# Kernel optimization log

Hardware: AMD Instinct MI355X
Metric: run time of the kernel (lower is better)

The kernel has to match this reference:

```python
import jax, jax.numpy as jnp
import numpy as np

NUM_HEADS = 16
TOP_K = 128
LN_EPS = 1e-5


def layernorm(x, w, b):
    mu = jnp.mean(x, axis=-1, keepdims=True)
    var = jnp.mean((x - mu) ** 2, axis=-1, keepdims=True)
    return (x - mu) * jax.lax.rsqrt(var + LN_EPS) * w + b


def top_k_activation(x, k):
    # keep top-k along last dim, zero elsewhere (scatter, like torch.scatter_)
    n = x.shape[-1]
    if k >= n:
        return x
    vals, idx = jax.lax.top_k(x, k)
    flat = x.reshape(-1, n)
    rows = jnp.arange(flat.shape[0])[:, None]
    out = jnp.zeros_like(flat).at[rows, idx.reshape(-1, k)].set(vals.reshape(-1, k))
    return out.reshape(x.shape)


def setup_inputs() -> dict:
    key = jax.random.key(0)
    ks = jax.random.split(key, 8)
    B, S, H = 2, 2048, 1024
    hd = H // NUM_HEADS
    return {
        "x": jax.random.normal(ks[0], (B, S, H), dtype=jnp.float32),
        "W_Q": jax.random.normal(ks[1], (H, H), dtype=jnp.float32) * 0.02,
        "W_K": jax.random.normal(ks[2], (H, H), dtype=jnp.float32) * 0.02,
        "W_V": jax.random.normal(ks[3], (H, H), dtype=jnp.float32) * 0.02,
        "W_O": jax.random.normal(ks[4], (H, H), dtype=jnp.float32) * 0.02,
        "q_ln_w": jnp.ones((hd,), dtype=jnp.float32),
        "q_ln_b": jnp.zeros((hd,), dtype=jnp.float32),
        "k_ln_w": jnp.ones((hd,), dtype=jnp.float32),
        "k_ln_b": jnp.zeros((hd,), dtype=jnp.float32),
        "sparse_W_V": jax.random.normal(ks[5], (NUM_HEADS, hd, TOP_K), dtype=jnp.float32) * 0.02,
        "sparse_W_O": jax.random.normal(ks[6], (NUM_HEADS, TOP_K, hd), dtype=jnp.float32) * 0.02,
    }


def reference(x, W_Q, W_K, W_V, W_O, q_ln_w, q_ln_b, k_ln_w, k_ln_b, sparse_W_V, sparse_W_O):
    B, S, H = x.shape
    nh = sparse_W_V.shape[0]
    hd = H // nh
    # projections (torch Linear: x @ W.T)
    def split_heads(t):
        return t.reshape(B, S, nh, hd).transpose(0, 2, 1, 3)  # [B, nh, S, hd]
    Q = split_heads(jnp.einsum('bsd,od->bso', x, W_Q))
    K = split_heads(jnp.einsum('bsd,od->bso', x, W_K))
    V = split_heads(jnp.einsum('bsd,od->bso', x, W_V))
    Q = layernorm(Q, q_ln_w, q_ln_b)
    K = layernorm(K, k_ln_w, k_ln_b)
    scores = jnp.einsum('bhqd,bhkd->bhqk', Q, K) / jnp.sqrt(jnp.float32(hd))
    attn = jax.nn.softmax(scores, axis=-1)
    context = jnp.einsum('bhqk,bhkd->bhqd', attn, V)  # [B, nh, S, hd]
    # faithful to source: transpose then reshape mixes batch/seq/head dims
    context_flat = context.transpose(0, 2, 1, 3).reshape(B * nh, S, hd)
    v_weights = sparse_W_V.mean(axis=2)  # [nh, hd]
    z = jnp.einsum('bnd,hd->bhn', context_flat, v_weights)  # [B*nh, nh, S]
    z_sparse = top_k_activation(z, TOP_K)  # top-k along seq axis, as in source
    o_weights = sparse_W_O.mean(axis=1)  # [nh, hd]
    y_flat = jnp.einsum('bhn,hd->bnd', z_sparse, o_weights)  # [B*nh, S, hd]
    y = y_flat.reshape(B, nh, S, hd).transpose(0, 2, 1, 3).reshape(B, S, H)
    y = jnp.einsum('bsd,od->bso', y, W_O)
    return y
```

## Files before the change

kernel.cpp:

```cpp
#include <hip/hip_runtime.h>
#include <math.h>

#define NB   2
#define SEQ  2048
#define NHD  16
#define HDD  64
#define HID  1024
#define TOPK 128

__global__ void k_prep_means(const float* __restrict__ sWV, const float* __restrict__ sWO,
                             double* __restrict__ vw, double* __restrict__ ow) {
  int t = threadIdx.x;
  for (int o = t; o < NHD * HDD; o += 256) {
    const float* p = sWV + (size_t)o * TOPK;
    double s = 0.0;
    for (int i = 0; i < TOPK; i++) s += (double)p[i];
    vw[o] = s * (1.0 / 128.0);
    int h = o >> 6, d = o & 63;
    const float* q = sWO + ((size_t)h * TOPK) * HDD + d;
    double s2 = 0.0;
    for (int i = 0; i < TOPK; i++) s2 += (double)q[(size_t)i * HDD];
    ow[o] = s2 * (1.0 / 128.0);
  }
}

__global__ void k_prep_wvp_g(const float* __restrict__ W_V, const float* __restrict__ W_O,
                             const double* __restrict__ vw, const double* __restrict__ ow,
                             double* __restrict__ WVP, float* __restrict__ G) {
  int blk = blockIdx.x;
  int t = threadIdx.x;
  if (blk < 256) {
    int n = blk >> 4, h = blk & 15;
    for (int j = t; j < HID; j += 256) {
      double s = 0.0;
      for (int d = 0; d < 64; d++)
        s += (double)W_V[(size_t)(n * 64 + d) * HID + j] * vw[h * 64 + d];
      WVP[(size_t)blk * HID + j] = s;
    }
  } else {
    int r = blk - 256;
    int m = r >> 4, h = r & 15;
    for (int o = t; o < HID; o += 256) {
      double s = 0.0;
      for (int d = 0; d < 64; d++)
        s += ow[h * 64 + d] * (double)W_O[(size_t)o * HID + m * 64 + d];
      G[(size_t)r * HID + o] = (float)s;
    }
  }
}

__global__ __launch_bounds__(256) void k_proj_qk(
    const float* __restrict__ x, const float* __restrict__ W_Q, const float* __restrict__ W_K,
    const float* __restrict__ qw, const float* __restrict__ qb,
    const float* __restrict__ kw, const float* __restrict__ kb,
    double* __restrict__ Qh, double* __restrict__ Kh) {
  __shared__ float  AsT[32][68];
  __shared__ float  BsT[32][68];
  __shared__ double Cs[64][65];
  __shared__ double red[64][4];

  int rt = blockIdx.x, ot = blockIdx.y;
  bool isQ = (ot < 16);
  const float* W = isQ ? W_Q : W_K;
  int head = isQ ? ot : ot - 16;
  int o0 = head * 64;
  int t = threadIdx.x;
  int tr = t >> 4, tc = t & 15;

  double acc[4][4];
  #pragma unroll
  for (int i = 0; i < 4; i++)
    #pragma unroll
    for (int j = 0; j < 4; j++) acc[i][j] = 0.0;

  for (int k0 = 0; k0 < HID; k0 += 32) {
    #pragma unroll
    for (int i = 0; i < 8; i++) {
      int idx = t + i * 256;
      int r = idx >> 5, c = idx & 31;
      AsT[c][r] = x[(size_t)(rt * 64 + r) * HID + k0 + c];
      BsT[c][r] = W[(size_t)(o0 + r) * HID + k0 + c];
    }
    __syncthreads();
    #pragma unroll 1
    for (int kk = 0; kk < 32; kk++) {
      float4 af = *(const float4*)&AsT[kk][tr * 4];
      float4 bf = *(const float4*)&BsT[kk][tc * 4];
      double a[4], b[4];
      a[0] = (double)af.x; a[1] = (double)af.y; a[2] = (double)af.z; a[3] = (double)af.w;
      b[0] = (double)bf.x; b[1] = (double)bf.y; b[2] = (double)bf.z; b[3] = (double)bf.w;
      #pragma unroll
      for (int i = 0; i < 4; i++)
        #pragma unroll
        for (int j = 0; j < 4; j++) acc[i][j] = fma(a[i], b[j], acc[i][j]);
    }
    __syncthreads();
  }

  #pragma unroll
  for (int i = 0; i < 4; i++)
    #pragma unroll
    for (int j = 0; j < 4; j++) Cs[tr * 4 + i][tc * 4 + j] = acc[i][j];
  __syncthreads();

  int r = t >> 2, p = t & 3;
  double s = 0.0;
  for (int i = 0; i < 16; i++) s += Cs[r][p * 16 + i];
  red[r][p] = s;
  __syncthreads();
  double mu = (red[r][0] + red[r][1] + red[r][2] + red[r][3]) * (1.0 / 64.0);
  __syncthreads();
  double s2 = 0.0;
  for (int i = 0; i < 16; i++) { double dl = Cs[r][p * 16 + i] - mu; s2 += dl * dl; }
  red[r][p] = s2;
  __syncthreads();
  double var = (red[r][0] + red[r][1] + red[r][2] + red[r][3]) * (1.0 / 64.0);
  double inv = 1.0 / sqrt(var + 1e-5);

  int R = rt * 64 + r;
  int b = R >> 11, ss = R & 2047;
  const float* lw = isQ ? qw : kw;
  const float* lb = isQ ? qb : kb;
  double* outp = isQ ? Qh : Kh;
  size_t base = (((size_t)b * 16 + head) * SEQ + ss) * 64;
  for (int i = 0; i < 16; i++) {
    int d = p * 16 + i;
    outp[base + d] = (Cs[r][d] - mu) * inv * (double)lw[d] + (double)lb[d];
  }
}

__global__ __launch_bounds__(256) void k_proj_vp(
    const float* __restrict__ x, const double* __restrict__ WVP, double* __restrict__ Vp) {
  __shared__ float  AsT[32][68];
  __shared__ double BsT[32][68];
  int rt = blockIdx.x, ot = blockIdx.y;
  int t = threadIdx.x, tr = t >> 4, tc = t & 15;

  double acc[4][4];
  #pragma unroll
  for (int i = 0; i < 4; i++)
    #pragma unroll
    for (int j = 0; j < 4; j++) acc[i][j] = 0.0;

  for (int k0 = 0; k0 < HID; k0 += 32) {
    #pragma unroll
    for (int i = 0; i < 8; i++) {
      int idx = t + i * 256;
      int r = idx >> 5, c = idx & 31;
      AsT[c][r] = x[(size_t)(rt * 64 + r) * HID + k0 + c];
      BsT[c][r] = WVP[(size_t)(ot * 64 + r) * HID + k0 + c];
    }
    __syncthreads();
    #pragma unroll 1
    for (int kk = 0; kk < 32; kk++) {
      float4 af = *(const float4*)&AsT[kk][tr * 4];
      double2 b01 = *(const double2*)&BsT[kk][tc * 4];
      double2 b23 = *(const double2*)&BsT[kk][tc * 4 + 2];
      double a[4], b[4];
      a[0] = (double)af.x; a[1] = (double)af.y; a[2] = (double)af.z; a[3] = (double)af.w;
      b[0] = b01.x; b[1] = b01.y; b[2] = b23.x; b[3] = b23.y;
      #pragma unroll
      for (int i = 0; i < 4; i++)
        #pragma unroll
        for (int j = 0; j < 4; j++) acc[i][j] = fma(a[i], b[j], acc[i][j]);
    }
    __syncthreads();
  }
  #pragma unroll
  for (int i = 0; i < 4; i++) {
    int R = rt * 64 + tr * 4 + i;
    int b = R >> 11, k = R & 2047;
    #pragma unroll
    for (int j = 0; j < 4; j++) {
      int cc = ot * 64 + tc * 4 + j;
      int n = cc >> 4, h = cc & 15;
      Vp[((((size_t)b * 16 + n) * SEQ) + k) * 16 + h] = acc[i][j];
    }
  }
}

__global__ __launch_bounds__(256, 2) void k_attn(
    const double* __restrict__ Qh, const double* __restrict__ Kh,
    const double* __restrict__ Vp, double* __restrict__ pnum, double* __restrict__ pden) {
  int kh = blockIdx.x;
  int qt = blockIdx.y;
  int bn = blockIdx.z;
  int t = threadIdx.x;
  int s = qt * 256 + t;
  int kspan = SEQ / gridDim.x;

  __shared__ double2 K2[64][32];
  __shared__ double2 V2[64][8];

  double2 q2[32];
  const double2* qp = (const double2*)(Qh + ((size_t)bn * SEQ + s) * 64);
  #pragma unroll
  for (int d = 0; d < 32; d++) q2[d] = qp[d];

  double2 num2[8];
  #pragma unroll
  for (int i = 0; i < 8; i++) { num2[i].x = 0.0; num2[i].y = 0.0; }
  double den = 0.0;

  int k0 = kh * kspan;
  for (int kc = 0; kc < kspan; kc += 64) {
    const double2* kb = (const double2*)(Kh + ((size_t)bn * SEQ + k0 + kc) * 64);
    #pragma unroll
    for (int i = 0; i < 8; i++) {
      int idx = t + i * 256;
      K2[idx >> 5][idx & 31] = kb[idx];
    }
    const double2* vb = (const double2*)(Vp + ((size_t)bn * SEQ + k0 + kc) * 16);
    #pragma unroll
    for (int i = 0; i < 2; i++) {
      int idx = t + i * 256;
      V2[idx >> 3][idx & 7] = vb[idx];
    }
    __syncthreads();
    #pragma unroll 1
    for (int kk = 0; kk < 64; kk += 4) {
      double s0 = 0.0, s1 = 0.0, s2 = 0.0, s3 = 0.0;
      #pragma unroll
      for (int d2 = 0; d2 < 32; d2++) {
        double2 qq = q2[d2];
        double2 k0v = K2[kk + 0][d2];
        double2 k1v = K2[kk + 1][d2];
        double2 k2v = K2[kk + 2][d2];
        double2 k3v = K2[kk + 3][d2];
        s0 = fma(qq.x, k0v.x, s0); s0 = fma(qq.y, k0v.y, s0);
        s1 = fma(qq.x, k1v.x, s1); s1 = fma(qq.y, k1v.y, s1);
        s2 = fma(qq.x, k2v.x, s2); s2 = fma(qq.y, k2v.y, s2);
        s3 = fma(qq.x, k3v.x, s3); s3 = fma(qq.y, k3v.y, s3);
      }
      double e0 = exp(s0 * 0.125);
      double e1 = exp(s1 * 0.125);
      double e2 = exp(s2 * 0.125);
      double e3 = exp(s3 * 0.125);
      den += (e0 + e1) + (e2 + e3);
      #pragma unroll
      for (int h2 = 0; h2 < 8; h2++) {
        double2 v0 = V2[kk + 0][h2];
        double2 v1 = V2[kk + 1][h2];
        double2 v2 = V2[kk + 2][h2];
        double2 v3 = V2[kk + 3][h2];
        double2 a = num2[h2];
        a.x = fma(e0, v0.x, a.x); a.x = fma(e1, v1.x, a.x);
        a.x = fma(e2, v2.x, a.x); a.x = fma(e3, v3.x, a.x);
        a.y = fma(e0, v0.y, a.y); a.y = fma(e1, v1.y, a.y);
        a.y = fma(e2, v2.y, a.y); a.y = fma(e3, v3.y, a.y);
        num2[h2] = a;
      }
    }
    __syncthreads();
  }
  size_t pb = ((size_t)kh * 32 + bn) * SEQ + s;
  pden[pb] = den;
  #pragma unroll
  for (int h2 = 0; h2 < 8; h2++) {
    pnum[pb * 16 + 2 * h2]     = num2[h2].x;
    pnum[pb * 16 + 2 * h2 + 1] = num2[h2].y;
  }
}

__global__ void k_combine(const double* __restrict__ pnum, const double* __restrict__ pden,
                          double* __restrict__ zrow, int nkh) {
  int id = blockIdx.x * 256 + threadIdx.x;
  int bn = id >> 11, s = id & 2047;
  int b = bn >> 4, n = bn & 15;
  double den = 0.0;
  for (int j = 0; j < nkh; j++) den += pden[(size_t)j * 65536 + id];
  int bp = b * 16 + (s >> 7);
  int np = ((s & 127) << 4) | n;
  for (int h = 0; h < 16; h++) {
    double nm = 0.0;
    for (int j = 0; j < nkh; j++) nm += pnum[((size_t)j * 65536 + id) * 16 + h];
    zrow[((size_t)bp * 16 + h) * 2048 + np] = nm / den;
  }
}

__device__ inline unsigned long long dkey(double v) {
  unsigned long long u = (unsigned long long)__double_as_longlong(v);
  return (u & 0x8000000000000000ULL) ? ~u : (u | 0x8000000000000000ULL);
}

__global__ __launch_bounds__(256) void k_topk(const double* __restrict__ zrow,
                                              float* __restrict__ zs) {
  int row = blockIdx.x;
  int t = threadIdx.x;
  const double* src = zrow + (size_t)row * 2048;
  double v[8];
  unsigned long long key[8];
  #pragma unroll
  for (int i = 0; i < 8; i++) { v[i] = src[t + i * 256]; key[i] = dkey(v[i]); }

  __shared__ unsigned sh_cnt[4];
  __shared__ unsigned sh_cg[4], sh_ce[4];
  int w = t >> 6, lane = t & 63;

  unsigned long long lo = 0ULL, hi = 0xFFFFFFFFFFFFFFFFULL;
  while (lo < hi) {
    unsigned long long mid = lo + ((hi - lo) >> 1);
    unsigned c = 0;
    #pragma unroll
    for (int i = 0; i < 8; i++) c += (key[i] > mid) ? 1u : 0u;
    for (int off = 32; off; off >>= 1) c += __shfl_down(c, off);
    if (lane == 0) sh_cnt[w] = c;
    __syncthreads();
    unsigned total = sh_cnt[0] + sh_cnt[1] + sh_cnt[2] + sh_cnt[3];
    __syncthreads();
    if (total < TOPK) hi = mid; else lo = mid + 1;
  }
  unsigned long long tau = lo;

  unsigned cg = 0, ce = 0;
  #pragma unroll
  for (int i = 0; i < 8; i++) {
    cg += (key[i] > tau) ? 1u : 0u;
    ce += (key[i] == tau) ? 1u : 0u;
  }
  for (int off = 32; off; off >>= 1) { cg += __shfl_down(cg, off); ce += __shfl_down(ce, off); }
  if (lane == 0) { sh_cg[w] = cg; sh_ce[w] = ce; }
  __syncthreads();
  unsigned c_gt = sh_cg[0] + sh_cg[1] + sh_cg[2] + sh_cg[3];
  unsigned c_eq = sh_ce[0] + sh_ce[1] + sh_ce[2] + sh_ce[3];
  unsigned need = TOPK - c_gt;

  unsigned idxThr = 2048;
  if (c_eq > need) {
    unsigned l2 = 0, h2 = 2048;
    while (l2 < h2) {
      unsigned m2 = (l2 + h2) >> 1;
      unsigned c = 0;
      #pragma unroll
      for (int i = 0; i < 8; i++) {
        unsigned idx = (unsigned)(t + i * 256);
        c += (key[i] == tau && idx < m2) ? 1u : 0u;
      }
      for (int off = 32; off; off >>= 1) c += __shfl_down(c, off);
      if (lane == 0) sh_cnt[w] = c;
      __syncthreads();
      unsigned tot = sh_cnt[0] + sh_cnt[1] + sh_cnt[2] + sh_cnt[3];
      __syncthreads();
      if (tot >= need) h2 = m2; else l2 = m2 + 1;
    }
    idxThr = l2;
  }

  float* dst = zs + (size_t)row * 2048;
  #pragma unroll
  for (int i = 0; i < 8; i++) {
    unsigned idx = (unsigned)(t + i * 256);
    bool keep = (key[i] > tau) ||
                (key[i] == tau && (c_eq <= need || idx < idxThr));
    dst[idx] = keep ? (float)v[i] : 0.0f;
  }
}

__global__ __launch_bounds__(256) void k_out(const float* __restrict__ zs,
                                             const float* __restrict__ G,
                                             float* __restrict__ out) {
  __shared__ float Al[64][65];
  __shared__ float Bl[64][65];
  int rt = blockIdx.x, ot = blockIdx.y;
  int t = threadIdx.x, tr = t >> 4, tc = t & 15;
  int Rb = rt * 64;
  int b = Rb >> 11, s0 = Rb & 2047;

  float acc[4][4];
  #pragma unroll
  for (int i = 0; i < 4; i++)
    #pragma unroll
    for (int j = 0; j < 4; j++) acc[i][j] = 0.0f;

  for (int kc = 0; kc < 256; kc += 64) {
    #pragma unroll
    for (int i = 0; i < 16; i++) {
      int idx = t + i * 256;
      int c = idx >> 6, r = idx & 63;
      int cc = kc + c;
      Al[r][c] = zs[(((size_t)(b * 16 + (cc >> 4))) * 16 + (cc & 15)) * 2048 + s0 + r];
      Bl[c][r] = G[(size_t)(kc + c) * HID + ot * 64 + r];
    }
    __syncthreads();
    #pragma unroll 1
    for (int kk = 0; kk < 64; kk++) {
      float a[4], bb[4];
      #pragma unroll
      for (int i = 0; i < 4; i++) a[i] = Al[tr * 4 + i][kk];
      #pragma unroll
      for (int j = 0; j < 4; j++) bb[j] = Bl[kk][tc * 4 + j];
      #pragma unroll
      for (int i = 0; i < 4; i++)
        #pragma unroll
        for (int j = 0; j < 4; j++) acc[i][j] = fmaf(a[i], bb[j], acc[i][j]);
    }
    __syncthreads();
  }
  #pragma unroll
  for (int i = 0; i < 4; i++) {
    int R = Rb + tr * 4 + i;
    #pragma unroll
    for (int j = 0; j < 4; j++)
      out[(size_t)R * HID + ot * 64 + tc * 4 + j] = acc[i][j];
  }
}

extern "C" void kernel_launch(void* const* d_in, const int* in_sizes, int n_in,
                              void* d_out, int out_size, void* d_ws, size_t ws_size,
                              hipStream_t stream) {
  const float* x   = (const float*)d_in[0];
  const float* W_Q = (const float*)d_in[1];
  const float* W_K = (const float*)d_in[2];
  const float* W_V = (const float*)d_in[3];
  const float* W_O = (const float*)d_in[4];
  const float* qw  = (const float*)d_in[5];
  const float* qb  = (const float*)d_in[6];
  const float* kw  = (const float*)d_in[7];
  const float* kb  = (const float*)d_in[8];
  const float* sWV = (const float*)d_in[9];
  const float* sWO = (const float*)d_in[10];
  float* out = (float*)d_out;
  char* ws = (char*)d_ws;

  const size_t NEED4 = 114311168ULL;
  int nkh = (ws_size >= NEED4) ? 4 : 2;

  double* Qh   = (double*)(ws + 0);
  double* Kh   = (double*)(ws + 33554432ULL);
  double* Vp   = (double*)(ws + 67108864ULL);
  double* WVP  = (double*)(ws + 75497472ULL);
  float*  G    = (float*) (ws + 77594624ULL);
  double* vw   = (double*)(ws + 78643200ULL);
  double* ow   = (double*)(ws + 78651392ULL);
  double* pnum = (double*)(ws + 78659584ULL);
  double* pden = (double*)(ws + 78659584ULL + (size_t)nkh * 8388608ULL);
  double* zrow = (double*)(ws + 0);
  float*  zs   = (float*) (ws + 8388608ULL);

  k_prep_means<<<dim3(1), dim3(256), 0, stream>>>(sWV, sWO, vw, ow);
  k_prep_wvp_g<<<dim3(512), dim3(256), 0, stream>>>(W_V, W_O, vw, ow, WVP, G);
  k_proj_qk<<<dim3(64, 32), dim3(256), 0, stream>>>(x, W_Q, W_K, qw, qb, kw, kb, Qh, Kh);
  k_proj_vp<<<dim3(64, 4), dim3(256), 0, stream>>>(x, WVP, Vp);
  k_attn<<<dim3(nkh, 8, 32), dim3(256), 0, stream>>>(Qh, Kh, Vp, pnum, pden);
  k_combine<<<dim3(256), dim3(256), 0, stream>>>(pnum, pden, zrow, nkh);
  k_topk<<<dim3(512), dim3(256), 0, stream>>>(zrow, zs);
  k_out<<<dim3(64, 16), dim3(256), 0, stream>>>(zs, G, out);
}
```

Baseline: 1.642 ms.

## Store projection tiles as row-major doubles and load attention K/V tiles directly to LDS

```diff
diff --git a/kernel.cpp b/kernel.cpp
--- a/kernel.cpp
+++ b/kernel.cpp
@@ -7,6 +7,12 @@
 #define HDD  64
 #define HID  1024
 #define TOPK 128
+
+__device__ __forceinline__ void gload_lds16(const void* g, void* l) {
+  __builtin_amdgcn_global_load_lds(
+      (__attribute__((address_space(1))) void*)g,
+      (__attribute__((address_space(3))) void*)l, 16, 0, 0);
+}
 
 __global__ void k_prep_means(const float* __restrict__ sWV, const float* __restrict__ sWO,
                              double* __restrict__ vw, double* __restrict__ ow) {
@@ -54,10 +60,11 @@
     const float* __restrict__ qw, const float* __restrict__ qb,
     const float* __restrict__ kw, const float* __restrict__ kb,
     double* __restrict__ Qh, double* __restrict__ Kh) {
-  __shared__ float  AsT[32][68];
-  __shared__ float  BsT[32][68];
-  __shared__ double Cs[64][65];
+  __shared__ double smem[4224];
   __shared__ double red[64][4];
+  double* As = smem;
+  double* Bs = smem + 2112;
+  double (*Cs)[65] = (double(*)[65])smem;
 
   int rt = blockIdx.x, ot = blockIdx.y;
   bool isQ = (ot < 16);
@@ -78,17 +85,17 @@
     for (int i = 0; i < 8; i++) {
       int idx = t + i * 256;
       int r = idx >> 5, c = idx & 31;
-      AsT[c][r] = x[(size_t)(rt * 64 + r) * HID + k0 + c];
-      BsT[c][r] = W[(size_t)(o0 + r) * HID + k0 + c];
+      As[r * 33 + c] = (double)x[(size_t)(rt * 64 + r) * HID + k0 + c];
+      Bs[r * 33 + c] = (double)W[(size_t)(o0 + r) * HID + k0 + c];
     }
     __syncthreads();
     #pragma unroll 1
     for (int kk = 0; kk < 32; kk++) {
-      float4 af = *(const float4*)&AsT[kk][tr * 4];
-      float4 bf = *(const float4*)&BsT[kk][tc * 4];
       double a[4], b[4];
-      a[0] = (double)af.x; a[1] = (double)af.y; a[2] = (double)af.z; a[3] = (double)af.w;
-      b[0] = (double)bf.x; b[1] = (double)bf.y; b[2] = (double)bf.z; b[3] = (double)bf.w;
+      #pragma unroll
+      for (int i = 0; i < 4; i++) a[i] = As[(tr * 4 + i) * 33 + kk];
+      #pragma unroll
+      for (int j = 0; j < 4; j++) b[j] = Bs[(tc * 4 + j) * 33 + kk];
       #pragma unroll
       for (int i = 0; i < 4; i++)
         #pragma unroll
@@ -131,8 +138,8 @@
 
 __global__ __launch_bounds__(256) void k_proj_vp(
     const float* __restrict__ x, const double* __restrict__ WVP, double* __restrict__ Vp) {
-  __shared__ float  AsT[32][68];
-  __shared__ double BsT[32][68];
+  __shared__ double As[64][33];
+  __shared__ double Bs[64][33];
   int rt = blockIdx.x, ot = blockIdx.y;
   int t = threadIdx.x, tr = t >> 4, tc = t & 15;
 
@@ -147,18 +154,17 @@
     for (int i = 0; i < 8; i++) {
       int idx = t + i * 256;
       int r = idx >> 5, c = idx & 31;
-      AsT[c][r] = x[(size_t)(rt * 64 + r) * HID + k0 + c];
-      BsT[c][r] = WVP[(size_t)(ot * 64 + r) * HID + k0 + c];
+      As[r][c] = (double)x[(size_t)(rt * 64 + r) * HID + k0 + c];
+      Bs[r][c] = WVP[(size_t)(ot * 64 + r) * HID + k0 + c];
     }
     __syncthreads();
     #pragma unroll 1
     for (int kk = 0; kk < 32; kk++) {
-      float4 af = *(const float4*)&AsT[kk][tr * 4];
-      double2 b01 = *(const double2*)&BsT[kk][tc * 4];
-      double2 b23 = *(const double2*)&BsT[kk][tc * 4 + 2];
       double a[4], b[4];
-      a[0] = (double)af.x; a[1] = (double)af.y; a[2] = (double)af.z; a[3] = (double)af.w;
-      b[0] = b01.x; b[1] = b01.y; b[2] = b23.x; b[3] = b23.y;
+      #pragma unroll
+      for (int i = 0; i < 4; i++) a[i] = As[tr * 4 + i][kk];
+      #pragma unroll
+      for (int j = 0; j < 4; j++) b[j] = Bs[tc * 4 + j][kk];
       #pragma unroll
       for (int i = 0; i < 4; i++)
         #pragma unroll
@@ -208,13 +214,13 @@
     #pragma unroll
     for (int i = 0; i < 8; i++) {
       int idx = t + i * 256;
-      K2[idx >> 5][idx & 31] = kb[idx];
+      gload_lds16(kb + idx, &K2[idx >> 5][idx & 31]);
     }
     const double2* vb = (const double2*)(Vp + ((size_t)bn * SEQ + k0 + kc) * 16);
     #pragma unroll
     for (int i = 0; i < 2; i++) {
       int idx = t + i * 256;
-      V2[idx >> 3][idx & 7] = vb[idx];
+      gload_lds16(vb + idx, &V2[idx >> 3][idx & 7]);
     }
     __syncthreads();
     #pragma unroll 1
```

New measurement: 2.299 ms. 40.1% more time.
